# Kernel optimization log

Measured on AMD Instinct MI355X. Metric: run time of the kernel, lower is better.

The kernel has to match this reference:

```python
import jax, jax.numpy as jnp
import numpy as np

N, INPUTDIM, OUTDIM, GRIDSIZE = 32768, 64, 256, 32


def setup_inputs() -> dict:
    key = jax.random.key(0)
    k1, k2 = jax.random.split(key)
    x = jax.random.normal(k1, (N, INPUTDIM), dtype=jnp.float32)
    # xavier_uniform over tensor of shape (2, outdim, inputdim, gridsize):
    # fan_in = inputdim*gridsize, fan_out = outdim*gridsize (torch treats dim0=fan_out-ish,
    # but exact init scale is irrelevant for correctness; use a matching uniform range)
    fan_in = INPUTDIM * GRIDSIZE
    fan_out = OUTDIM * GRIDSIZE
    bound = float(np.sqrt(6.0 / (fan_in + fan_out)))
    fouriercoeffs = jax.random.uniform(
        k2, (2, OUTDIM, INPUTDIM, GRIDSIZE), dtype=jnp.float32,
        minval=-bound, maxval=bound)
    bias = jnp.zeros((1, OUTDIM), dtype=jnp.float32)
    return {"x": x, "fouriercoeffs": fouriercoeffs, "bias": bias}


def reference(x, fouriercoeffs, bias):
    # gridsize_param rounds back to GRIDSIZE at init -> static.
    g = fouriercoeffs.shape[-1]
    k = jnp.arange(1, g + 1, dtype=x.dtype)  # (g,)
    # Fourier feature expansion: (N, inputdim, g)
    xk = x[:, :, None] * k[None, None, :]
    c = jnp.cos(xk)
    s = jnp.sin(xk)
    # Contract over (inputdim, gridsize) -> two GEMMs over flattened dim
    y = jnp.einsum('nig,oig->no', c, fouriercoeffs[0])
    y = y + jnp.einsum('nig,oig->no', s, fouriercoeffs[1])
    y = y + bias  # (1, outdim) broadcasts over N
    return y
```

## Files before the change

kernel.cpp:

```cpp
#include <hip/hip_runtime.h>


#define IDIM 64
#define ODIM 256
#define KDIM 4096
#define BM 128

typedef __attribute__((ext_vector_type(8))) unsigned short ushort8_t;
typedef __bf16 bf16x8 __attribute__((ext_vector_type(8)));
typedef float floatx4 __attribute__((ext_vector_type(4)));

__device__ __forceinline__ unsigned short f2bf_rne(float f) {
  unsigned int u = __float_as_uint(f);
  return (unsigned short)((u + 0x7FFFu + ((u >> 16) & 1u)) >> 16);
}

__global__ void __launch_bounds__(256) wconv(const float* __restrict__ fc,
                                             unsigned short* __restrict__ Wr) {
  int t = blockIdx.x * 256 + threadIdx.x;
  int lane = t & 63;
  int j = (t >> 6) & 7;
  int bb = t >> 9;
  int wn2 = bb & 1;
  int wk = (bb >> 1) & 1;
  int kt = bb >> 2;
  int o = wn2 * 128 + j * 16 + (lane & 15);
  int g0 = (lane >> 4) * 8;
  const float* src = fc + ((size_t)wk << 19) + o * 2048 + kt * 32 + g0;
  const float4 v0 = *(const float4*)(src);
  const float4 v1 = *(const float4*)(src + 4);
  ushort8_t r;
  r[0] = f2bf_rne(v0.x);
  r[1] = f2bf_rne(v0.y);
  r[2] = f2bf_rne(v0.z);
  r[3] = f2bf_rne(v0.w);
  r[4] = f2bf_rne(v1.x);
  r[5] = f2bf_rne(v1.y);
  r[6] = f2bf_rne(v1.z);
  r[7] = f2bf_rne(v1.w);
  *(ushort8_t*)(Wr + (size_t)t * 8) = r;
}

__global__ void __launch_bounds__(512, 2) fkan_gemm(const float* __restrict__ X,
                                                    const unsigned short* __restrict__ Wr,
                                                    const float* __restrict__ bias,
                                                    float* __restrict__ out) {
  __shared__ __align__(16) unsigned short As[2][8192];
  __shared__ __align__(16) float red[64 * 260];

  const int t = threadIdx.x;
  const int wv = t >> 6;
  const int ln = t & 63;
  const int lm = ln & 15;
  const int quad = ln >> 4;
  const int wk = wv & 1;
  const int wn2 = (wv >> 1) & 1;
  const int wm2 = wv >> 2;
  const int m0 = blockIdx.x * BM;

  const int arow = t >> 2;
  const int q = t & 3;
  const float g0f = (float)(8 * q + 1);

  const int ga_c = arow * 8 + (q ^ (arow & 7));
  const int ga_s = arow * 8 + ((4 + q) ^ (arow & 7));

  const unsigned short* const bwave = Wr + (size_t)(wk * 2 + wn2) * 4096 + ln * 8;

  floatx4 acc[4][8];
#pragma unroll
  for (int a = 0; a < 4; ++a)
#pragma unroll
    for (int b = 0; b < 8; ++b)
      acc[a][b] = (floatx4){0.0f, 0.0f, 0.0f, 0.0f};

  const float* xptr = X + (size_t)(m0 + arow) * IDIM;

  auto features = [&](float xv, int buf) {
    const float inv2pi = 0.15915494309189535f;
    float u = xv * inv2pi;
    float u0 = u * g0f;
    float c1 = __builtin_amdgcn_cosf(u);
    float s1 = __builtin_amdgcn_sinf(u);
    float C = __builtin_amdgcn_cosf(u0);
    float S = __builtin_amdgcn_sinf(u0);
    bf16x8 cb, sb;
    cb[0] = (__bf16)C;
    sb[0] = (__bf16)S;
#pragma unroll
    for (int jj = 1; jj < 8; ++jj) {
      float Cn = __builtin_fmaf(C, c1, -(S * s1));
      float Sn = __builtin_fmaf(S, c1, (C * s1));
      C = Cn;
      S = Sn;
      cb[jj] = (__bf16)C;
      sb[jj] = (__bf16)S;
    }
    ushort8_t* As8 = (ushort8_t*)As[buf];
    As8[ga_c] = __builtin_bit_cast(ushort8_t, cb);
    As8[ga_s] = __builtin_bit_cast(ushort8_t, sb);
  };

  bf16x8 breg[8];

  auto ktstep = [&](int ktn, int cur, int nxt) {
    float xn = xptr[ktn];
    const ushort8_t* A8 = (const ushort8_t*)As[cur];
    const int ch = wk * 4 + quad;
    bf16x8 af[4];
#pragma unroll
    for (int mt = 0; mt < 4; ++mt) {
      int r = wm2 * 64 + mt * 16 + lm;
      af[mt] = __builtin_bit_cast(bf16x8, A8[r * 8 + (ch ^ (r & 7))]);
    }
    const unsigned short* bn = bwave + (size_t)ktn * 16384;

    __builtin_amdgcn_s_setprio(1);
#pragma unroll
    for (int nt = 0; nt < 8; ++nt) {
#pragma unroll
      for (int mt = 0; mt < 4; ++mt)
        acc[mt][nt] = __builtin_amdgcn_mfma_f32_16x16x32_bf16(
            af[mt], breg[nt], acc[mt][nt], 0, 0, 0);
      breg[nt] = __builtin_bit_cast(bf16x8, *(const ushort8_t*)(bn + nt * 512));
    }
    __builtin_amdgcn_s_setprio(0);

    features(xn, nxt);
    __syncthreads();
  };

  auto ktlast = [&](int cur) {
    const ushort8_t* A8 = (const ushort8_t*)As[cur];
    const int ch = wk * 4 + quad;
    bf16x8 af[4];
#pragma unroll
    for (int mt = 0; mt < 4; ++mt) {
      int r = wm2 * 64 + mt * 16 + lm;
      af[mt] = __builtin_bit_cast(bf16x8, A8[r * 8 + (ch ^ (r & 7))]);
    }
    __builtin_amdgcn_s_setprio(1);
#pragma unroll
    for (int nt = 0; nt < 8; ++nt)
#pragma unroll
      for (int mt = 0; mt < 4; ++mt)
        acc[mt][nt] = __builtin_amdgcn_mfma_f32_16x16x32_bf16(
            af[mt], breg[nt], acc[mt][nt], 0, 0, 0);
    __builtin_amdgcn_s_setprio(0);
  };

#pragma unroll
  for (int nt = 0; nt < 8; ++nt)
    breg[nt] = __builtin_bit_cast(bf16x8, *(const ushort8_t*)(bwave + nt * 512));
  features(xptr[0], 0);
  __syncthreads();

  for (int kt = 0; kt < 62; kt += 2) {
    ktstep(kt + 1, 0, 1);
    ktstep(kt + 2, 1, 0);
  }
  ktstep(63, 0, 1);
  ktlast(1);

  for (int half = 0; half < 2; ++half) {
    __syncthreads();
    if (wk == 1 && wm2 == half) {
#pragma unroll
      for (int mt = 0; mt < 4; ++mt)
#pragma unroll
        for (int nt = 0; nt < 8; ++nt) {
          int col = wn2 * 128 + nt * 16 + lm;
#pragma unroll
          for (int idx = 0; idx < 4; ++idx)
            red[(mt * 16 + quad * 4 + idx) * 260 + col] = acc[mt][nt][idx];
        }
    }
    __syncthreads();
    if (wk == 0 && wm2 == half) {
#pragma unroll
      for (int nt = 0; nt < 8; ++nt) {
        int col = wn2 * 128 + nt * 16 + lm;
        float bv = bias[col];
#pragma unroll
        for (int mt = 0; mt < 4; ++mt) {
          int rbase = m0 + half * 64 + mt * 16 + quad * 4;
#pragma unroll
          for (int idx = 0; idx < 4; ++idx)
            out[(size_t)(rbase + idx) * ODIM + col] =
                acc[mt][nt][idx] + red[(mt * 16 + quad * 4 + idx) * 260 + col] + bv;
        }
      }
    }
  }
}

extern "C" void kernel_launch(void* const* d_in, const int* in_sizes, int n_in,
                              void* d_out, int out_size, void* d_ws, size_t ws_size,
                              hipStream_t stream) {
  const float* x = (const float*)d_in[0];
  const float* fc = (const float*)d_in[1];
  const float* bias = (const float*)d_in[2];
  float* out = (float*)d_out;
  unsigned short* Wr = (unsigned short*)d_ws;

  hipLaunchKernelGGL(wconv, dim3(512), dim3(256), 0, stream, fc, Wr);
  hipLaunchKernelGGL(fkan_gemm, dim3(256), dim3(512), 0, stream, x, Wr, bias, out);
}
```

Before: 132.6 us.

## Compute Fourier A-fragments in registers per wave, dropping LDS feature buffers

Stages the block's X tile once, transposed into shared memory. Each wave then computes its own cos or sin bf16 fragments directly in registers, in MFMA operand layout, instead of writing features to double-buffered LDS and reading them back. This removes the per-k-step __syncthreads and the LDS write/read traffic, and software-pipelines feature computation with the MFMA cluster. The cost is redundant transcendental work: each wave recomputes features for 4 rows across the wn2 split, which duplicates work and adds register pressure.

Measured after the change: 154.2 us. 1.16x slower.

```diff
diff --git a/kernel.cpp b/kernel.cpp
--- a/kernel.cpp
+++ b/kernel.cpp
@@ -45,8 +45,9 @@
                                                     const unsigned short* __restrict__ Wr,
                                                     const float* __restrict__ bias,
                                                     float* __restrict__ out) {
-  __shared__ __align__(16) unsigned short As[2][8192];
-  __shared__ __align__(16) float red[64 * 260];
+  __shared__ __align__(16) unsigned char smem[66560];
+  float* const Xt = (float*)smem;
+  float* const red = (float*)smem;
 
   const int t = threadIdx.x;
   const int wv = t >> 6;
@@ -58,14 +59,23 @@
   const int wm2 = wv >> 2;
   const int m0 = blockIdx.x * BM;
 
-  const int arow = t >> 2;
-  const int q = t & 3;
-  const float g0f = (float)(8 * q + 1);
-
-  const int ga_c = arow * 8 + (q ^ (arow & 7));
-  const int ga_s = arow * 8 + ((4 + q) ^ (arow & 7));
+  {
+    int row = t >> 2;
+    int ks = (t & 3) * 16;
+    const float* src = X + (size_t)(m0 + row) * IDIM + ks;
+#pragma unroll
+    for (int j = 0; j < 4; ++j) {
+      float4 v = *(const float4*)(src + j * 4);
+      Xt[(ks + j * 4 + 0) * 128 + row] = v.x;
+      Xt[(ks + j * 4 + 1) * 128 + row] = v.y;
+      Xt[(ks + j * 4 + 2) * 128 + row] = v.z;
+      Xt[(ks + j * 4 + 3) * 128 + row] = v.w;
+    }
+  }
 
   const unsigned short* const bwave = Wr + (size_t)(wk * 2 + wn2) * 4096 + ln * 8;
+  const float g0q = (float)(8 * quad + 1);
+  const int xoff = wm2 * 64 + lm;
 
   floatx4 acc[4][8];
 #pragma unroll
@@ -74,47 +84,56 @@
     for (int b = 0; b < 8; ++b)
       acc[a][b] = (floatx4){0.0f, 0.0f, 0.0f, 0.0f};
 
-  const float* xptr = X + (size_t)(m0 + arow) * IDIM;
-
-  auto features = [&](float xv, int buf) {
+  __syncthreads();
+
+  auto xread = [&](int k, float* xv) {
+    const float* p = Xt + k * 128 + xoff;
+    xv[0] = p[0];
+    xv[1] = p[16];
+    xv[2] = p[32];
+    xv[3] = p[48];
+  };
+
+  auto compA = [&](const float* xv, bf16x8* af) {
     const float inv2pi = 0.15915494309189535f;
-    float u = xv * inv2pi;
-    float u0 = u * g0f;
-    float c1 = __builtin_amdgcn_cosf(u);
-    float s1 = __builtin_amdgcn_sinf(u);
-    float C = __builtin_amdgcn_cosf(u0);
-    float S = __builtin_amdgcn_sinf(u0);
-    bf16x8 cb, sb;
-    cb[0] = (__bf16)C;
-    sb[0] = (__bf16)S;
-#pragma unroll
-    for (int jj = 1; jj < 8; ++jj) {
-      float Cn = __builtin_fmaf(C, c1, -(S * s1));
-      float Sn = __builtin_fmaf(S, c1, (C * s1));
-      C = Cn;
-      S = Sn;
-      cb[jj] = (__bf16)C;
-      sb[jj] = (__bf16)S;
-    }
-    ushort8_t* As8 = (ushort8_t*)As[buf];
-    As8[ga_c] = __builtin_bit_cast(ushort8_t, cb);
-    As8[ga_s] = __builtin_bit_cast(ushort8_t, sb);
+#pragma unroll
+    for (int mt = 0; mt < 4; ++mt) {
+      float u = xv[mt] * inv2pi;
+      float u0 = u * g0q;
+      float c1 = __builtin_amdgcn_cosf(u);
+      float s1 = __builtin_amdgcn_sinf(u);
+      float C = __builtin_amdgcn_cosf(u0);
+      float S = __builtin_amdgcn_sinf(u0);
+      bf16x8 fb;
+      if (wk == 0) {
+        fb[0] = (__bf16)C;
+#pragma unroll
+        for (int j = 1; j < 8; ++j) {
+          float Cn = __builtin_fmaf(C, c1, -(S * s1));
+          float Sn = __builtin_fmaf(S, c1, (C * s1));
+          C = Cn;
+          S = Sn;
+          fb[j] = (__bf16)C;
+        }
+      } else {
+        fb[0] = (__bf16)S;
+#pragma unroll
+        for (int j = 1; j < 8; ++j) {
+          float Cn = __builtin_fmaf(C, c1, -(S * s1));
+          float Sn = __builtin_fmaf(S, c1, (C * s1));
+          C = Cn;
+          S = Sn;
+          fb[j] = (__bf16)S;
+        }
+      }
+      af[mt] = fb;
+    }
   };
 
   bf16x8 breg[8];
 
-  auto ktstep = [&](int ktn, int cur, int nxt) {
-    float xn = xptr[ktn];
-    const ushort8_t* A8 = (const ushort8_t*)As[cur];
-    const int ch = wk * 4 + quad;
-    bf16x8 af[4];
-#pragma unroll
-    for (int mt = 0; mt < 4; ++mt) {
-      int r = wm2 * 64 + mt * 16 + lm;
-      af[mt] = __builtin_bit_cast(bf16x8, A8[r * 8 + (ch ^ (r & 7))]);
-    }
-    const unsigned short* bn = bwave + (size_t)ktn * 16384;
-
+  auto mcluster = [&](bf16x8* af, int reload_kt, bool do_reload) {
+    const unsigned short* bn = bwave + (size_t)reload_kt * 16384;
     __builtin_amdgcn_s_setprio(1);
 #pragma unroll
     for (int nt = 0; nt < 8; ++nt) {
@@ -122,45 +141,32 @@
       for (int mt = 0; mt < 4; ++mt)
         acc[mt][nt] = __builtin_amdgcn_mfma_f32_16x16x32_bf16(
             af[mt], breg[nt], acc[mt][nt], 0, 0, 0);
-      breg[nt] = __builtin_bit_cast(bf16x8, *(const ushort8_t*)(bn + nt * 512));
-    }
-    __builtin_amdgcn_s_setprio(0);
-
-    features(xn, nxt);
-    __syncthreads();
-  };
-
-  auto ktlast = [&](int cur) {
-    const ushort8_t* A8 = (const ushort8_t*)As[cur];
-    const int ch = wk * 4 + quad;
-    bf16x8 af[4];
-#pragma unroll
-    for (int mt = 0; mt < 4; ++mt) {
-      int r = wm2 * 64 + mt * 16 + lm;
-      af[mt] = __builtin_bit_cast(bf16x8, A8[r * 8 + (ch ^ (r & 7))]);
-    }
-    __builtin_amdgcn_s_setprio(1);
-#pragma unroll
-    for (int nt = 0; nt < 8; ++nt)
-#pragma unroll
-      for (int mt = 0; mt < 4; ++mt)
-        acc[mt][nt] = __builtin_amdgcn_mfma_f32_16x16x32_bf16(
-            af[mt], breg[nt], acc[mt][nt], 0, 0, 0);
+      if (do_reload)
+        breg[nt] = __builtin_bit_cast(bf16x8, *(const ushort8_t*)(bn + nt * 512));
+    }
     __builtin_amdgcn_s_setprio(0);
   };
 
+  float xA[4], xB[4], x0[4];
+  bf16x8 afA[4], afB[4];
 #pragma unroll
   for (int nt = 0; nt < 8; ++nt)
     breg[nt] = __builtin_bit_cast(bf16x8, *(const ushort8_t*)(bwave + nt * 512));
-  features(xptr[0], 0);
-  __syncthreads();
+  xread(0, x0);
+  compA(x0, afA);
+  xread(1, xA);
 
   for (int kt = 0; kt < 62; kt += 2) {
-    ktstep(kt + 1, 0, 1);
-    ktstep(kt + 2, 1, 0);
+    xread(kt + 2, xB);
+    compA(xA, afB);
+    mcluster(afA, kt + 1, true);
+    xread(kt + 3, xA);
+    compA(xB, afA);
+    mcluster(afB, kt + 2, true);
   }
-  ktstep(63, 0, 1);
-  ktlast(1);
+  compA(xA, afB);
+  mcluster(afA, 63, true);
+  mcluster(afB, 0, false);
 
   for (int half = 0; half < 2; ++half) {
     __syncthreads();
```
